# Kernel optimization log

Measured on AMD Instinct MI355X. Metric: run time of the kernel, lower is better.

The kernel has to match this reference:

```python
import jax, jax.numpy as jnp
import numpy as np

B, TE, TD, H = 8, 512, 256, 256  # batch, enc len, dec len, hidden (He==Hd)

def setup_inputs() -> dict:
    key = jax.random.key(0)
    k1, k2, k3, k4, k5 = jax.random.split(key, 5)
    # Keras 'uniform' initializer: U(-0.05, 0.05)
    u = lambda k, s: jax.random.uniform(k, s, jnp.float32, -0.05, 0.05)
    return {
        "encoder_out_seq": jax.random.normal(k1, (B, TE, H), jnp.float32),
        "decoder_out_seq": jax.random.normal(k2, (B, TD, H), jnp.float32),
        "W_a": u(k3, (H, H)),
        "U_a": u(k4, (H, H)),
        "V_a": u(k5, (H, 1)),
    }

def reference(encoder_out_seq, decoder_out_seq, W_a, U_a, V_a):
    # Bahdanau additive attention, fully batched (same math as the per-step K.rnn loop)
    We = jnp.einsum('bih,hk->bik', encoder_out_seq, W_a)   # [B,Te,H]
    Uh = jnp.einsum('bjh,hk->bjk', decoder_out_seq, U_a)   # [B,Td,H]
    # energies: V_a^T tanh(We_i + Uh_j)  -> [B,Td,Te]
    t = jnp.tanh(We[:, None, :, :] + Uh[:, :, None, :])    # [B,Td,Te,H]
    e = jnp.einsum('bjih,h->bji', t, V_a[:, 0])             # [B,Td,Te]
    e = jax.nn.softmax(e, axis=-1)                          # softmax over encoder positions
    c = jnp.einsum('bji,bih->bjh', e, encoder_out_seq)      # [B,Td,H]
    return (c, e)
```

## Files before the change

### kernel.cpp

```cpp
#include <hip/hip_runtime.h>


#define BB 8
#define TE 512
#define TD 256
#define HH 256

#define EXP2F(x) __builtin_amdgcn_exp2f(x)
#define RCPF(x)  __builtin_amdgcn_rcpf(x)
#define KSCALE   2.8853900817779268f
#define NSC      (-2.8853900817779268f)

typedef __attribute__((ext_vector_type(8))) short short8_t;
typedef __attribute__((ext_vector_type(4))) float f32x4;

__device__ __forceinline__ unsigned short f2bf(float x) {
    unsigned int u = __float_as_uint(x);
    return (unsigned short)((u + 0x7FFFu + ((u >> 16) & 1u)) >> 16);
}
__device__ __forceinline__ float bf2f(unsigned short h) {
    return __uint_as_float(((unsigned int)h) << 16);
}

__global__ __launch_bounds__(256) void k_tw(
    const float* __restrict__ Wa, const float* __restrict__ Ua,
    unsigned short* __restrict__ Wth, unsigned short* __restrict__ Wtl)
{
    const int t    = threadIdx.x;
    const int s    = blockIdx.x >> 4;
    const int tile = blockIdx.x & 15;
    const int tk   = (tile >> 2) * 64;
    const int th   = (tile & 3) * 64;
    const float* W = s ? Ua : Wa;

    __shared__ float Ls[64][65];
    const int kr = t >> 4;
    const int hc = (t & 15) * 4;
    #pragma unroll
    for (int r = 0; r < 4; r++) {
        float4 v = *(const float4*)(W + (size_t)(tk + kr + 16 * r) * HH + th + hc);
        Ls[kr + 16 * r][hc + 0] = v.x; Ls[kr + 16 * r][hc + 1] = v.y;
        Ls[kr + 16 * r][hc + 2] = v.z; Ls[kr + 16 * r][hc + 3] = v.w;
    }
    __syncthreads();
    const int hr  = t >> 4;
    const int kc4 = (t & 15) * 4;
    #pragma unroll
    for (int r = 0; r < 4; r++) {
        const int hl = hr + 16 * r;
        float f0 = Ls[kc4 + 0][hl], f1 = Ls[kc4 + 1][hl];
        float f2 = Ls[kc4 + 2][hl], f3 = Ls[kc4 + 3][hl];
        ushort4 hi, lo;
        hi.x = f2bf(f0); lo.x = f2bf(f0 - bf2f(hi.x));
        hi.y = f2bf(f1); lo.y = f2bf(f1 - bf2f(hi.y));
        hi.z = f2bf(f2); lo.z = f2bf(f2 - bf2f(hi.z));
        hi.w = f2bf(f3); lo.w = f2bf(f3 - bf2f(hi.w));
        const size_t o = ((size_t)(s * 256 + th + hl)) * 256 + tk + kc4;
        *(ushort4*)(Wth + o) = hi;
        *(ushort4*)(Wtl + o) = lo;
    }
}

__global__ __launch_bounds__(256) void k_pre(
    const float* __restrict__ enc, const float* __restrict__ dec,
    const unsigned short* __restrict__ Wth, const unsigned short* __restrict__ Wtl,
    float* __restrict__ W4, float* __restrict__ Uhe)
{
    const int t  = threadIdx.x;
    const int it = blockIdx.x >> 2;
    const int ht = blockIdx.x & 3;
    const int i0 = it * 64;
    const int h0 = ht * 64;
    const bool is_enc = (i0 < BB * TE);
    const float* X = is_enc ? (enc + (size_t)i0 * HH)
                            : (dec + (size_t)(i0 - BB * TE) * HH);
    const int s = is_enc ? 0 : 1;
    const unsigned short* Ah = Wth + ((size_t)(s * 256 + h0)) * 256;
    const unsigned short* Al = Wtl + ((size_t)(s * 256 + h0)) * 256;

    __shared__ unsigned short At_h[64][40], At_l[64][40];
    __shared__ unsigned short Xs_h[64][40], Xs_l[64][40];

    const int sr = t >> 2;
    const int sq = (t & 3) * 8;

    const int wv = t >> 6, l = t & 63;
    const int wh = (wv & 1) * 32;
    const int wi = (wv >> 1) * 32;
    const int fr = l & 15;
    const int fk = (l >> 4) * 8;
    const int rq = l >> 4;

    f32x4 acc[2][2];
    #pragma unroll
    for (int a0 = 0; a0 < 2; a0++)
        #pragma unroll
        for (int a1 = 0; a1 < 2; a1++)
            acc[a0][a1] = (f32x4){0.f, 0.f, 0.f, 0.f};

    short8_t aH = *(const short8_t*)(Ah + (size_t)sr * 256 + sq);
    short8_t aL = *(const short8_t*)(Al + (size_t)sr * 256 + sq);
    float4   x0 = *(const float4*)(X + (size_t)sr * HH + sq);
    float4   x1 = *(const float4*)(X + (size_t)sr * HH + sq + 4);

    #pragma unroll
    for (int c = 0; c < 8; c++) {
        short8_t xh, xl;
        {
            unsigned short h;
            h = f2bf(x0.x); xh[0] = (short)h; xl[0] = (short)f2bf(x0.x - bf2f(h));
            h = f2bf(x0.y); xh[1] = (short)h; xl[1] = (short)f2bf(x0.y - bf2f(h));
            h = f2bf(x0.z); xh[2] = (short)h; xl[2] = (short)f2bf(x0.z - bf2f(h));
            h = f2bf(x0.w); xh[3] = (short)h; xl[3] = (short)f2bf(x0.w - bf2f(h));
            h = f2bf(x1.x); xh[4] = (short)h; xl[4] = (short)f2bf(x1.x - bf2f(h));
            h = f2bf(x1.y); xh[5] = (short)h; xl[5] = (short)f2bf(x1.y - bf2f(h));
            h = f2bf(x1.z); xh[6] = (short)h; xl[6] = (short)f2bf(x1.z - bf2f(h));
            h = f2bf(x1.w); xh[7] = (short)h; xl[7] = (short)f2bf(x1.w - bf2f(h));
        }
        __syncthreads();
        *(short8_t*)&At_h[sr][sq] = aH;
        *(short8_t*)&At_l[sr][sq] = aL;
        *(short8_t*)&Xs_h[sr][sq] = xh;
        *(short8_t*)&Xs_l[sr][sq] = xl;
        if (c < 7) {
            const int kc = (c + 1) * 32;
            aH = *(const short8_t*)(Ah + (size_t)sr * 256 + kc + sq);
            aL = *(const short8_t*)(Al + (size_t)sr * 256 + kc + sq);
            x0 = *(const float4*)(X + (size_t)sr * HH + kc + sq);
            x1 = *(const float4*)(X + (size_t)sr * HH + kc + sq + 4);
        }
        __syncthreads();
        #pragma unroll
        for (int fm = 0; fm < 2; fm++) {
            short8_t a_h = *(const short8_t*)&At_h[wh + 16 * fm + fr][fk];
            short8_t a_l = *(const short8_t*)&At_l[wh + 16 * fm + fr][fk];
            #pragma unroll
            for (int fn = 0; fn < 2; fn++) {
                short8_t b_h = *(const short8_t*)&Xs_h[wi + 16 * fn + fr][fk];
                short8_t b_l = *(const short8_t*)&Xs_l[wi + 16 * fn + fr][fk];
                acc[fm][fn] = __builtin_amdgcn_mfma_f32_16x16x32_bf16(a_h, b_h, acc[fm][fn], 0, 0, 0);
                acc[fm][fn] = __builtin_amdgcn_mfma_f32_16x16x32_bf16(a_h, b_l, acc[fm][fn], 0, 0, 0);
                acc[fm][fn] = __builtin_amdgcn_mfma_f32_16x16x32_bf16(a_l, b_h, acc[fm][fn], 0, 0, 0);
            }
        }
    }

    #pragma unroll
    for (int fm = 0; fm < 2; fm++) {
        #pragma unroll
        for (int fn = 0; fn < 2; fn++) {
            f32x4 v = acc[fm][fn];
            float4 o;
            o.x = EXP2F(v[0] * KSCALE);
            o.y = EXP2F(v[1] * KSCALE);
            o.z = EXP2F(v[2] * KSCALE);
            o.w = EXP2F(v[3] * KSCALE);
            const int ig = i0 + wi + 16 * fn + fr;
            const int hb = h0 + wh + 16 * fm + rq * 4;
            if (is_enc) {
                const int b  = ig >> 9;
                const int ib = ig & 511;
                const int hq = hb >> 2;
                *(float4*)(W4 + (((size_t)b * 64 + hq) * TE + ib) * 4) = o;
            } else {
                const int j = ig - BB * TE;
                *(float4*)(Uhe + (size_t)j * HH + hb) = o;
            }
        }
    }
}

__global__ __launch_bounds__(512) void k_attn(
    const float* __restrict__ enc, const float* __restrict__ W4,
    const float* __restrict__ Uhe, const float* __restrict__ Va,
    float* __restrict__ out_c, float* __restrict__ out_e)
{
    const int wv = threadIdx.x >> 6, lane = threadIdx.x & 63;
    const int b   = blockIdx.x & 7;
    const int j0  = (blockIdx.x >> 3) * 4;
    const int jj0 = b * TD + j0;

    __shared__ float sP[4][TE];
    __shared__ float sR[8][4][HH];

    const int i = (wv << 6) + lane;
    const float* wp = W4 + ((size_t)b * 64 * TE + i) * 4;
    const float* ua = Uhe + (size_t)jj0 * HH;
    const float* va = Va;

    float a0 = 0.f, a1 = 0.f, a2 = 0.f, a3 = 0.f;

#define QSTEP(ACC, U)                                                     \
    {                                                                     \
        float A_ = fmaf(w4.x, (U).x, 1.f);                                \
        float B_ = fmaf(w4.y, (U).y, 1.f);                                \
        float C_ = fmaf(w4.z, (U).z, 1.f);                                \
        float D_ = fmaf(w4.w, (U).w, 1.f);                                \
        float dAB = A_ * B_, dCD = C_ * D_;                               \
        float nAB = fmaf(v4.x, B_, v4.y * A_);                            \
        float nCD = fmaf(v4.z, D_, v4.w * C_);                            \
        float num = fmaf(nAB, dCD, nCD * dAB);                            \
        ACC = fmaf(num, RCPF(dAB * dCD), ACC);                            \
    }

    #pragma unroll 2
    for (int q = 0; q < 64; q++) {
        float4 w4 = *(const float4*)(wp + (size_t)q * TE * 4);
        float4 v4 = *(const float4*)(va + 4 * q);
        float4 u0 = *(const float4*)(ua + 4 * q);
        float4 u1 = *(const float4*)(ua + HH + 4 * q);
        float4 u2 = *(const float4*)(ua + 2 * HH + 4 * q);
        float4 u3 = *(const float4*)(ua + 3 * HH + 4 * q);
        QSTEP(a0, u0)
        QSTEP(a1, u1)
        QSTEP(a2, u2)
        QSTEP(a3, u3)
    }
#undef QSTEP

    sP[0][i] = NSC * a0;
    sP[1][i] = NSC * a1;
    sP[2][i] = NSC * a2;
    sP[3][i] = NSC * a3;
    __syncthreads();

    if (wv < 4) {
        float ev[8];
        float m = -3.0e38f;
        #pragma unroll
        for (int k = 0; k < 8; k++) {
            ev[k] = sP[wv][lane + 64 * k];
            m = fmaxf(m, ev[k]);
        }
        #pragma unroll
        for (int off = 32; off; off >>= 1) m = fmaxf(m, __shfl_xor(m, off, 64));
        float s = 0.f;
        #pragma unroll
        for (int k = 0; k < 8; k++) { ev[k] = EXP2F(ev[k] - m); s += ev[k]; }
        #pragma unroll
        for (int off = 32; off; off >>= 1) s += __shfl_xor(s, off, 64);
        float rs = RCPF(s);
        float* oe = out_e + (size_t)(jj0 + wv) * TE;
        #pragma unroll
        for (int k = 0; k < 8; k++) {
            float p = ev[k] * rs;
            sP[wv][lane + 64 * k] = p;
            oe[lane + 64 * k] = p;
        }
    }
    __syncthreads();

    const int ib = wv << 6;
    const float* eb = enc + ((size_t)b * TE + ib) * HH + 4 * lane;
    float4 c0 = {0,0,0,0}, c1 = {0,0,0,0}, c2 = {0,0,0,0}, c3 = {0,0,0,0};
    #pragma unroll 2
    for (int k = 0; k < 64; k++) {
        float p0 = sP[0][ib + k];
        float p1 = sP[1][ib + k];
        float p2 = sP[2][ib + k];
        float p3 = sP[3][ib + k];
        float4 q = *(const float4*)(eb + (size_t)k * HH);
        c0.x = fmaf(p0, q.x, c0.x); c0.y = fmaf(p0, q.y, c0.y);
        c0.z = fmaf(p0, q.z, c0.z); c0.w = fmaf(p0, q.w, c0.w);
        c1.x = fmaf(p1, q.x, c1.x); c1.y = fmaf(p1, q.y, c1.y);
        c1.z = fmaf(p1, q.z, c1.z); c1.w = fmaf(p1, q.w, c1.w);
        c2.x = fmaf(p2, q.x, c2.x); c2.y = fmaf(p2, q.y, c2.y);
        c2.z = fmaf(p2, q.z, c2.z); c2.w = fmaf(p2, q.w, c2.w);
        c3.x = fmaf(p3, q.x, c3.x); c3.y = fmaf(p3, q.y, c3.y);
        c3.z = fmaf(p3, q.z, c3.z); c3.w = fmaf(p3, q.w, c3.w);
    }
    *(float4*)&sR[wv][0][4 * lane] = c0;
    *(float4*)&sR[wv][1][4 * lane] = c1;
    *(float4*)&sR[wv][2][4 * lane] = c2;
    *(float4*)&sR[wv][3][4 * lane] = c3;
    __syncthreads();

    {
        const int jr = wv & 3;
        const int h2 = (wv >> 2) * 128 + 2 * lane;
        float sx = 0.f, sy = 0.f;
        #pragma unroll
        for (int ww = 0; ww < 8; ww++) {
            float2 t = *(const float2*)&sR[ww][jr][h2];
            sx += t.x; sy += t.y;
        }
        float2 o; o.x = sx; o.y = sy;
        *(float2*)(out_c + (size_t)(jj0 + jr) * HH + h2) = o;
    }
}

extern "C" void kernel_launch(void* const* d_in, const int* in_sizes, int n_in,
                              void* d_out, int out_size, void* d_ws, size_t ws_size,
                              hipStream_t stream) {
    const float* enc = (const float*)d_in[0];
    const float* dec = (const float*)d_in[1];
    const float* Wa  = (const float*)d_in[2];
    const float* Ua  = (const float*)d_in[3];
    const float* Va  = (const float*)d_in[4];

    float* W4  = (float*)d_ws;
    float* Uhe = W4 + (size_t)BB * HH * TE;
    unsigned short* Wth = (unsigned short*)(Uhe + (size_t)BB * TD * HH);
    unsigned short* Wtl = Wth + 2 * 256 * 256;

    float* out_c = (float*)d_out;
    float* out_e = out_c + (size_t)BB * TD * HH;

    k_tw<<<32, 256, 0, stream>>>(Wa, Ua, Wth, Wtl);
    k_pre<<<384, 256, 0, stream>>>(enc, dec, Wth, Wtl, W4, Uhe);
    k_attn<<<BB * TD / 4, 512, 0, stream>>>(enc, W4, Uhe, Va, out_c, out_e);
}
```

Before: 107.9 us.

## Split attention kernel into energy and softmax-context kernels via workspace

Splits the fused attention kernel in two. The first kernel computes the energy scores with 256-thread blocks, each covering half of the encoder positions, and writes them to a global workspace buffer. The second kernel loads them into shared memory and does the softmax and context reduction. The intent is more independent blocks and better occupancy for the compute-heavy energy loop, which is also unrolled further. The cost is an extra launch plus a round trip of the energy matrix through global memory.

```diff
diff --git a/kernel.cpp b/kernel.cpp
--- a/kernel.cpp
+++ b/kernel.cpp
@@ -170,20 +170,17 @@
     }
 }
 
-__global__ __launch_bounds__(512) void k_attn(
-    const float* __restrict__ enc, const float* __restrict__ W4,
-    const float* __restrict__ Uhe, const float* __restrict__ Va,
-    float* __restrict__ out_c, float* __restrict__ out_e)
+__global__ __launch_bounds__(256) void k_energy(
+    const float* __restrict__ W4, const float* __restrict__ Uhe,
+    const float* __restrict__ Va, float* __restrict__ E)
 {
-    const int wv = threadIdx.x >> 6, lane = threadIdx.x & 63;
-    const int b   = blockIdx.x & 7;
-    const int j0  = (blockIdx.x >> 3) * 4;
-    const int jj0 = b * TD + j0;
-
-    __shared__ float sP[4][TE];
-    __shared__ float sR[8][4][HH];
-
-    const int i = (wv << 6) + lane;
+    const int t  = threadIdx.x;
+    const int b  = blockIdx.x & 7;
+    const int jg = (blockIdx.x >> 3) & 63;
+    const int ih = blockIdx.x >> 9;
+    const int jj0 = b * TD + jg * 4;
+    const int i   = ih * 256 + t;
+
     const float* wp = W4 + ((size_t)b * 64 * TE + i) * 4;
     const float* ua = Uhe + (size_t)jj0 * HH;
     const float* va = Va;
@@ -203,7 +200,7 @@
         ACC = fmaf(num, RCPF(dAB * dCD), ACC);                            \
     }
 
-    #pragma unroll 2
+    #pragma unroll 4
     for (int q = 0; q < 64; q++) {
         float4 w4 = *(const float4*)(wp + (size_t)q * TE * 4);
         float4 v4 = *(const float4*)(va + 4 * q);
@@ -218,10 +215,31 @@
     }
 #undef QSTEP
 
-    sP[0][i] = NSC * a0;
-    sP[1][i] = NSC * a1;
-    sP[2][i] = NSC * a2;
-    sP[3][i] = NSC * a3;
+    float* ep = E + (size_t)jj0 * TE + i;
+    ep[0]          = NSC * a0;
+    ep[TE]         = NSC * a1;
+    ep[2 * TE]     = NSC * a2;
+    ep[3 * TE]     = NSC * a3;
+}
+
+__global__ __launch_bounds__(512) void k_soft(
+    const float* __restrict__ enc, const float* __restrict__ E,
+    float* __restrict__ out_c, float* __restrict__ out_e)
+{
+    const int t  = threadIdx.x;
+    const int wv = t >> 6, lane = t & 63;
+    const int b   = blockIdx.x & 7;
+    const int j0  = (blockIdx.x >> 3) * 4;
+    const int jj0 = b * TD + j0;
+
+    __shared__ float sP[4][TE];
+    __shared__ float sR[8][4][HH];
+
+    {
+        const float* ep = E + (size_t)jj0 * TE;
+        float4 v = *(const float4*)(ep + t * 4);
+        *(float4*)&((float*)sP)[t * 4] = v;
+    }
     __syncthreads();
 
     if (wv < 4) {
@@ -281,8 +299,8 @@
         float sx = 0.f, sy = 0.f;
         #pragma unroll
         for (int ww = 0; ww < 8; ww++) {
-            float2 t = *(const float2*)&sR[ww][jr][h2];
-            sx += t.x; sy += t.y;
+            float2 tv = *(const float2*)&sR[ww][jr][h2];
+            sx += tv.x; sy += tv.y;
         }
         float2 o; o.x = sx; o.y = sy;
         *(float2*)(out_c + (size_t)(jj0 + jr) * HH + h2) = o;
@@ -302,11 +320,13 @@
     float* Uhe = W4 + (size_t)BB * HH * TE;
     unsigned short* Wth = (unsigned short*)(Uhe + (size_t)BB * TD * HH);
     unsigned short* Wtl = Wth + 2 * 256 * 256;
+    float* Ew = (float*)(Wtl + 2 * 256 * 256);
 
     float* out_c = (float*)d_out;
     float* out_e = out_c + (size_t)BB * TD * HH;
 
     k_tw<<<32, 256, 0, stream>>>(Wa, Ua, Wth, Wtl);
     k_pre<<<384, 256, 0, stream>>>(enc, dec, Wth, Wtl, W4, Uhe);
-    k_attn<<<BB * TD / 4, 512, 0, stream>>>(enc, W4, Uhe, Va, out_c, out_e);
-}
+    k_energy<<<BB * 64 * 2, 256, 0, stream>>>(W4, Uhe, Va, Ew);
+    k_soft<<<BB * TD / 4, 512, 0, stream>>>(enc, Ew, out_c, out_e);
+}
```

Measured after the change: 112.9 us. +4.7%, slower.
